# Performance work log

Measured on AMD Instinct MI355X. Metric: run time of the kernel, lower is better.

The kernel has to match this reference:

```python
import math
import jax, jax.numpy as jnp
import numpy as np

B, T, HIDDEN = 2, 2048, 1024
H, HKV, D = 16, 16, 64


def _rope_tables(T, D):
    inv_freq = 1.0 / (10000.0 ** (jnp.arange(0, D, 2, dtype=jnp.float32) / D))
    t = jnp.arange(T, dtype=jnp.float32)
    freqs = jnp.outer(t, inv_freq)               # [T, D/2]
    emb = jnp.concatenate([freqs, freqs], axis=-1)  # [T, D]
    return jnp.cos(emb), jnp.sin(emb)


def setup_inputs() -> dict:
    key = jax.random.key(0)
    k1, k2, k3 = jax.random.split(key, 3)
    hidden_states = jax.random.normal(k1, (B, T, HIDDEN), dtype=jnp.float32)
    cos, sin = _rope_tables(T, D)
    # trunc-normal-ish init, std = 1/sqrt(fan_in)
    w_qkv = jax.random.normal(k2, ((H + 2 * HKV) * D, HIDDEN), dtype=jnp.float32) / math.sqrt(HIDDEN)
    w_o = jax.random.normal(k3, (HIDDEN, H * D), dtype=jnp.float32) / math.sqrt(H * D)
    return {"hidden_states": hidden_states, "cos": cos, "sin": sin, "w_qkv": w_qkv, "w_o": w_o}


def _rotate_half(x):
    x1, x2 = jnp.split(x, 2, axis=-1)
    return jnp.concatenate([-x2, x1], axis=-1)


def reference(hidden_states, cos, sin, w_qkv, w_o):
    b, t, _ = hidden_states.shape
    # fused QKV projection: [B,T,(H+2*HKV)*D]
    qkv = jnp.einsum('bti,oi->bto', hidden_states, w_qkv)
    qkv = qkv.reshape(b, t, H + 2 * HKV, D)
    q = qkv[:, :, :H]                    # [B,T,H,D]
    k = qkv[:, :, H:H + HKV]             # [B,T,HKV,D]
    v = qkv[:, :, H + HKV:]              # [B,T,HKV,D]
    # inline RoPE; cos/sin broadcast over heads
    c = cos[:, None, :]
    s = sin[:, None, :]
    q = q * c + _rotate_half(q) * s
    k = k * c + _rotate_half(k) * s
    scale = 1.0 / math.sqrt(D)
    attn_scores = jnp.einsum('bthd,bThd->bhtT', q, k) * scale  # [B,H,T,T]
    mask = jnp.tril(jnp.ones((t, t), dtype=bool))
    attn_scores = jnp.where(mask[None, None, :, :], attn_scores, -1e9)
    attn = jax.nn.softmax(attn_scores, axis=-1)
    context = jnp.einsum('bhtT,bThd->bthd', attn, v).reshape(b, t, H * D)
    return jnp.einsum('bti,oi->bto', context, w_o)
```

## Files before the change

kernel.cpp:

```cpp
#include <hip/hip_runtime.h>

typedef __bf16 bf16_t;
typedef __bf16 bf16x4 __attribute__((ext_vector_type(4)));
typedef __bf16 bf16x8 __attribute__((ext_vector_type(8)));
typedef float f32x4 __attribute__((ext_vector_type(4)));
typedef unsigned int u32x2 __attribute__((ext_vector_type(2)));
typedef unsigned long long u64;

#define MFMA16(a, b, c) __builtin_amdgcn_mfma_f32_16x16x32_bf16((a), (b), (c), 0, 0, 0)

#define LDG2LDS16(g, l)                                                        \
    __builtin_amdgcn_global_load_lds(                                          \
        (const __attribute__((address_space(1))) void*)(g),                    \
        (__attribute__((address_space(3))) void*)(l), 16, 0, 0)

#if __has_builtin(__builtin_amdgcn_exp2f)
#define EXP2(x) __builtin_amdgcn_exp2f(x)
#else
#define EXP2(x) exp2f(x)
#endif

__device__ inline bf16x8 load8(const float* p) {
    const f32x4 a = *(const f32x4*)p;
    const f32x4 b = *(const f32x4*)(p + 4);
    bf16x8 r;
#pragma unroll
    for (int i = 0; i < 4; i++) { r[i] = (bf16_t)a[i]; r[4 + i] = (bf16_t)b[i]; }
    return r;
}

__device__ inline u32x2 as2(bf16x4 v) {
    u32x2 r;
    __builtin_memcpy(&r, &v, 8);
    return r;
}

__device__ inline bf16x4 shfl4(bf16x4 v, int src) {
    u64 x;
    __builtin_memcpy(&x, &v, 8);
    x = __shfl(x, src, 64);
    bf16x4 r;
    __builtin_memcpy(&r, &x, 8);
    return r;
}

__device__ inline bf16x8 p2pf(bf16x4 pb0, bf16x4 pb1, int quad, int lr) {
    bf16x8 pf;
#if __has_builtin(__builtin_amdgcn_permlane16_swap) && \
    __has_builtin(__builtin_amdgcn_permlane32_swap)
    const u32x2 P0 = as2(pb0);
    const u32x2 P1 = as2(pb1);
    const u32x2 s1a = __builtin_amdgcn_permlane16_swap(P0[0], P0[1], false, false);
    const u32x2 s1b = __builtin_amdgcn_permlane16_swap(P1[0], P1[1], false, false);
    const u32x2 s2a = __builtin_amdgcn_permlane32_swap(s1a[0], s1b[0], false, false);
    const u32x2 s2b = __builtin_amdgcn_permlane32_swap(s1a[1], s1b[1], false, false);
    const u32x2 s3a = __builtin_amdgcn_permlane16_swap(s2a[0], s2a[1], false, false);
    const u32x2 s3b = __builtin_amdgcn_permlane16_swap(s2b[0], s2b[1], false, false);
    const unsigned pfd[4] = {s3a[0], s3a[1], s3b[0], s3b[1]};
    __builtin_memcpy(&pf, pfd, 16);
#else
    const int srcLow = ((quad & 1) << 5) + lr;
    const int srcHigh = srcLow + 16;
    const bool loSel = (quad < 2);
    const bf16x4 a0 = shfl4(pb0, srcLow);
    const bf16x4 a1 = shfl4(pb1, srcLow);
    const bf16x4 b0 = shfl4(pb0, srcHigh);
    const bf16x4 b1 = shfl4(pb1, srcHigh);
    const bf16x4 lo = loSel ? a0 : a1;
    const bf16x4 hi = loSel ? b0 : b1;
#pragma unroll
    for (int r = 0; r < 4; r++) { pf[r] = lo[r]; pf[4 + r] = hi[r]; }
#endif
    return pf;
}

__global__ __launch_bounds__(256) void convert_kernel(const float* __restrict__ hs,
                                                      const float* __restrict__ wqkv,
                                                      const float* __restrict__ wo,
                                                      bf16_t* __restrict__ outb) {
    const size_t c = ((size_t)blockIdx.x * 256 + threadIdx.x) * 8;
    const float* src;
    size_t off;
    if (c < 4194304) { src = hs; off = c; }
    else if (c < 7340032) { src = wqkv; off = c - 4194304; }
    else { src = wo; off = c - 7340032; }
    *(bf16x8*)(outb + c) = load8(src + off);
}


template <int MODE, int NDIM, int BM>
__global__ __launch_bounds__(256) void gemm_bt(const bf16_t* __restrict__ A,
                                               const bf16_t* __restrict__ B,
                                               float* __restrict__ outp,
                                               bf16_t* __restrict__ q_ws,
                                               bf16_t* __restrict__ k_ws,
                                               bf16_t* __restrict__ v_ws,
                                               const float* __restrict__ cosb,
                                               const float* __restrict__ sinb) {
    constexpr int K = 1024;
    constexpr int IM = BM / 32;
    __shared__ __align__(16) bf16_t As[BM * 32];
    __shared__ __align__(16) bf16_t Bs[128 * 32];

    const int tid = threadIdx.x;
    const int w = tid >> 6;
    const int lane = tid & 63;
    const int lr = lane & 15;
    const int quad = lane >> 4;
    const int m0 = blockIdx.y * BM;
    const int n0 = blockIdx.x * 128;
    const int wm = (w & 1) * (BM / 2);
    const int wn = (w >> 1) * 64;

    const int srow = tid >> 2;
    const int skk = (((tid & 3) ^ ((tid >> 3) & 3)) * 8);
    const bf16_t* gA0 = A + (size_t)(m0 + srow) * K + skk;
    const bf16_t* gA1 = gA0 + (size_t)64 * K;
    const bf16_t* gB0 = B + (size_t)(n0 + srow) * K + skk;
    const bf16_t* gB1 = gB0 + (size_t)64 * K;
    bf16_t* lA0 = As + w * 512;
    bf16_t* lA1 = As + 2048 + w * 512;
    bf16_t* lB0 = Bs + w * 512;
    bf16_t* lB1 = Bs + 2048 + w * 512;

    const int qsw = (quad ^ ((lr >> 1) & 3)) * 8;

    f32x4 acc[IM][4] = {};

    for (int k0 = 0; k0 < K; k0 += 32) {
        LDG2LDS16(gA0 + k0, lA0);
        if constexpr (BM == 128) LDG2LDS16(gA1 + k0, lA1);
        LDG2LDS16(gB0 + k0, lB0);
        LDG2LDS16(gB1 + k0, lB1);
        __syncthreads();

        bf16x8 af[IM], bfm[4];
#pragma unroll
        for (int im = 0; im < IM; im++)
            af[im] = *(const bf16x8*)&As[(wm + im * 16 + lr) * 32 + qsw];
#pragma unroll
        for (int in = 0; in < 4; in++)
            bfm[in] = *(const bf16x8*)&Bs[(wn + in * 16 + lr) * 32 + qsw];
#pragma unroll
        for (int im = 0; im < IM; im++)
#pragma unroll
            for (int in = 0; in < 4; in++)
                acc[im][in] = MFMA16(af[im], bfm[in], acc[im][in]);
        __syncthreads();
    }

    if constexpr (MODE == 0) {
#pragma unroll
        for (int im = 0; im < IM; im++)
#pragma unroll
            for (int in = 0; in < 4; in++)
#pragma unroll
                for (int r = 0; r < 4; r++) {
                    const int m = m0 + wm + im * 16 + quad * 4 + r;
                    const int n = n0 + wn + in * 16 + lr;
                    outp[(size_t)m * NDIM + n] = acc[im][in][r];
                }
    } else {
        const int j = (n0 + wn) >> 6;
        if (j < 32) {
            const bool isq = (j < 16);
            const float qs = 0.125f * 1.44269504089f;
#pragma unroll
            for (int im = 0; im < IM; im++) {
#pragma unroll
                for (int r = 0; r < 4; r++) {
                    const int m = m0 + wm + im * 16 + quad * 4 + r;
                    const int b = m >> 11;
                    const int t = m & 2047;
#pragma unroll
                    for (int in = 0; in < 2; in++) {
                        const int d = in * 16 + lr;
                        const float x1 = acc[im][in][r];
                        const float x2 = acc[im][in + 2][r];
                        const float c = cosb[t * 64 + d];
                        const float s = sinb[t * 64 + d];
                        float y1 = x1 * c - x2 * s;
                        float y2 = x2 * c + x1 * s;
                        if (isq) {
                            y1 *= qs; y2 *= qs;
                            const size_t base =
                                ((size_t)(b * 16 + j) * 2048 + t) * 64 + d;
                            q_ws[base] = (bf16_t)y1;
                            q_ws[base + 32] = (bf16_t)y2;
                        } else {
                            const int bh = b * 16 + (j - 16);
                            const size_t off =
                                ((size_t)(bh * 128 + (t >> 4)) * 2) * 512 +
                                ((t & 15) + (d >> 3) * 16) * 8 + (d & 7);
                            k_ws[off] = (bf16_t)y1;
                            k_ws[off + 512] = (bf16_t)y2;
                        }
                    }
                }
            }
        } else {
#pragma unroll
            for (int im = 0; im < IM; im++)
#pragma unroll
                for (int in = 0; in < 4; in++)
#pragma unroll
                    for (int r = 0; r < 4; r++) {
                        const int m = m0 + wm + im * 16 + quad * 4 + r;
                        const int b = m >> 11;
                        const int t = m & 2047;
                        const int d = in * 16 + lr;
                        const int bh = b * 16 + (j - 32);
                        const size_t off =
                            ((size_t)(bh * 64 + (t >> 5)) * 4 + (d >> 4)) * 512 +
                            ((d & 15) + ((t & 31) >> 3) * 16) * 8 + (t & 7);
                        v_ws[off] = (bf16_t)acc[im][in][r];
                    }
        }
    }
}

__global__ __launch_bounds__(512, 4) void attn_kernel(const bf16_t* __restrict__ q_ws,
                                                      const bf16_t* __restrict__ k_ws,
                                                      const bf16_t* __restrict__ v_ws,
                                                      bf16_t* __restrict__ ctx) {
    __shared__ __align__(16) bf16_t Ks[2][4096];
    __shared__ __align__(16) bf16_t Vs[2][4096];

    const int tid = threadIdx.x;
    const int w = tid >> 6;
    const int wq = w & 3;
    const int lane = tid & 63;
    const int lr = lane & 15;
    const int quad = lane >> 4;
    const int bh = blockIdx.x & 31;
    const int g = blockIdx.x >> 5;
    const int pr = (g < 8) ? g : 23 - g;
    const int qtA = pr;
    const int qtB = 31 - pr;
    const int qtw = (w < 4) ? qtA : qtB;
    const int b = bh >> 4;
    const int hd = bh & 15;

    const bf16_t* kws = k_ws + (size_t)bh * 131072;
    const bf16_t* vws = v_ws + (size_t)bh * 131072;
    const int soff = wq * 512 + lane * 8;
    const int lo8 = lane * 8;

    bf16x8 ones8;
#pragma unroll
    for (int i = 0; i < 8; i++) ones8[i] = (bf16_t)1.0f;

#define ASTAGE(kb, bufi)                                                       \
    {                                                                          \
        if (w < 4) {                                                           \
            LDG2LDS16(kws + (size_t)(kb) * 4096 + soff, &Ks[bufi][wq * 512]);  \
            LDG2LDS16(kws + (size_t)(kb) * 4096 + 2048 + soff,                 \
                      &Ks[bufi][2048 + wq * 512]);                             \
        } else {                                                               \
            LDG2LDS16(vws + (size_t)(kb) * 4096 + soff, &Vs[bufi][wq * 512]);  \
            LDG2LDS16(vws + (size_t)(kb) * 4096 + 2048 + soff,                 \
                      &Vs[bufi][2048 + wq * 512]);                             \
        }                                                                      \
    }

    const int trow = qtw * 64 + wq * 16;
    const int query = trow + lr;

    const bf16_t* qb = q_ws + ((size_t)bh * 2048 + trow + lr) * 64 + quad * 8;
    const bf16x8 qlo = *(const bf16x8*)qb;
    const bf16x8 qhi = *(const bf16x8*)(qb + 32);

    f32x4 o[4] = {};
    f32x4 lacc = {};

    ASTAGE(0, 0);
    asm volatile("s_waitcnt vmcnt(0)" ::: "memory");
    __builtin_amdgcn_s_barrier();
    asm volatile("" ::: "memory");

    for (int kb = 0; kb <= qtB; kb++) {
        const int bufi = kb & 1;
        if (kb < qtB) ASTAGE(kb + 1, bufi ^ 1);

        if (kb <= qtw) {
            f32x4 s[4];
#pragma unroll
            for (int n = 0; n < 4; n++) {
                const bf16x8 k0 = *(const bf16x8*)&Ks[bufi][(2 * n) * 512 + lo8];
                const bf16x8 k1 =
                    *(const bf16x8*)&Ks[bufi][(2 * n + 1) * 512 + lo8];
                const f32x4 z = {};
                s[n] = MFMA16(k0, qlo, z);
                s[n] = MFMA16(k1, qhi, s[n]);
            }

            const int u0 = kb * 64;
            if (kb == qtw) {
#pragma unroll
                for (int n = 0; n < 4; n++)
#pragma unroll
                    for (int r = 0; r < 4; r++)
                        if (u0 + n * 16 + quad * 4 + r > query) s[n][r] = -1e9f;
            }

            bf16x4 pb[4];
#pragma unroll
            for (int n = 0; n < 4; n++)
#pragma unroll
                for (int r = 0; r < 4; r++) pb[n][r] = (bf16_t)EXP2(s[n][r]);

#pragma unroll
            for (int hh = 0; hh < 2; hh++) {
                const bf16x8 pf = p2pf(pb[2 * hh], pb[2 * hh + 1], quad, lr);
                lacc = MFMA16(ones8, pf, lacc);
#pragma unroll
                for (int n = 0; n < 4; n++) {
                    const bf16x8 vvf =
                        *(const bf16x8*)&Vs[bufi][(hh * 4 + n) * 512 + lo8];
                    o[n] = MFMA16(vvf, pf, o[n]);
                }
            }
        }

        asm volatile("s_waitcnt lgkmcnt(0) vmcnt(0)" ::: "memory");
        __builtin_amdgcn_s_barrier();
        asm volatile("" ::: "memory");
    }

    const float inv = 1.0f / fmaxf(lacc[0], 1e-30f);
    const size_t base = ((size_t)b * 2048 + query) * 1024 + hd * 64 + quad * 4;
#pragma unroll
    for (int n = 0; n < 4; n++) {
        bf16x4 ob;
#pragma unroll
        for (int r = 0; r < 4; r++) ob[r] = (bf16_t)(o[n][r] * inv);
        *(bf16x4*)&ctx[base + n * 16] = ob;
    }
#undef ASTAGE
}

extern "C" void kernel_launch(void* const* d_in, const int* in_sizes, int n_in,
                              void* d_out, int out_size, void* d_ws, size_t ws_size,
                              hipStream_t stream) {
    const float* hs = (const float*)d_in[0];
    const float* cosb = (const float*)d_in[1];
    const float* sinb = (const float*)d_in[2];
    const float* wqkv = (const float*)d_in[3];
    const float* wo = (const float*)d_in[4];
    float* out = (float*)d_out;

    char* ws = (char*)d_ws;
    bf16_t* hs_b = (bf16_t*)(ws);
    bf16_t* wqkv_b = hs_b + 4194304;
    bf16_t* wo_b = hs_b + 7340032;
    bf16_t* q_ws = (bf16_t*)(ws + (size_t)(16u << 20));
    bf16_t* k_ws = (bf16_t*)(ws + (size_t)(24u << 20));
    bf16_t* v_ws = (bf16_t*)(ws + (size_t)(32u << 20));
    bf16_t* ctx = (bf16_t*)(ws);

    const dim3 blk(256);

    convert_kernel<<<dim3(4096), blk, 0, stream>>>(hs, wqkv, wo, hs_b);

    gemm_bt<1, 3072, 128><<<dim3(24, 32), blk, 0, stream>>>(
        hs_b, wqkv_b, nullptr, q_ws, k_ws, v_ws, cosb, sinb);

    attn_kernel<<<dim3(512), dim3(512), 0, stream>>>(q_ws, k_ws, v_ws, ctx);

    gemm_bt<0, 1024, 64><<<dim3(8, 64), blk, 0, stream>>>(
        ctx, wo_b, out, nullptr, nullptr, nullptr, nullptr, nullptr);
}
```

Measured before the change: 164.8 us.

## Replace QKV GEMM with 512-thread K64 double-buffered async-LDS kernel

Adds a dedicated QKV projection kernel that uses 512 threads, a K-step of 64, and double-buffered global-to-LDS direct loads with XOR-swizzled shared memory and explicit waitcnt/barrier scheduling. Loads for tile t+2 are issued while computing tile t, and MFMA issue is raised in priority with setprio. The goal is to hide global memory latency and halve the number of barrier iterations compared with the old K32 single-buffered GEMM. The cost is more LDS per block (64 KB), which may limit occupancy. The old MODE 1 epilogue is removed from the generic template.

```diff
diff --git a/kernel.cpp b/kernel.cpp
--- a/kernel.cpp
+++ b/kernel.cpp
@@ -88,6 +88,161 @@
 }
 
 
+__global__ __launch_bounds__(512, 4) void gemm1_k64(const bf16_t* __restrict__ A,
+                                                    const bf16_t* __restrict__ B,
+                                                    bf16_t* __restrict__ q_ws,
+                                                    bf16_t* __restrict__ k_ws,
+                                                    bf16_t* __restrict__ v_ws,
+                                                    const float* __restrict__ cosb,
+                                                    const float* __restrict__ sinb) {
+    constexpr int K = 1024;
+    __shared__ __align__(16) bf16_t As[16384];
+    __shared__ __align__(16) bf16_t Bs[16384];
+
+    const int tid = threadIdx.x;
+    const int w = tid >> 6;
+    const int lane = tid & 63;
+    const int lr = lane & 15;
+    const int quad = lane >> 4;
+    const int m0 = blockIdx.y * 128;
+    const int n0 = blockIdx.x * 128;
+    const int wm = (w & 3) * 32;
+    const int wn = (w >> 2) * 64;
+
+    const int trow = tid >> 3;
+    const int slot = (tid & 7) ^ (trow & 7);
+    const bf16_t* gA = A + (size_t)(m0 + trow) * K + slot * 8;
+    const bf16_t* gB = B + (size_t)(n0 + trow) * K + slot * 8;
+
+#define G1STAGE(t, b)                                                          \
+    {                                                                          \
+        LDG2LDS16(gA + (size_t)(t) * 64, As + (b) * 8192 + w * 512);           \
+        LDG2LDS16(gA + (size_t)64 * K + (size_t)(t) * 64,                      \
+                  As + (b) * 8192 + 4096 + w * 512);                           \
+        LDG2LDS16(gB + (size_t)(t) * 64, Bs + (b) * 8192 + w * 512);           \
+        LDG2LDS16(gB + (size_t)64 * K + (size_t)(t) * 64,                      \
+                  Bs + (b) * 8192 + 4096 + w * 512);                           \
+    }
+
+    const int o0 = (quad ^ (lr & 7)) * 16;
+    const char* AbB = (const char*)As + (wm + lr) * 128;
+    const char* BbB = (const char*)Bs + (wn + lr) * 128;
+
+    f32x4 acc[2][4] = {};
+
+    G1STAGE(0, 0);
+    G1STAGE(1, 1);
+    asm volatile("s_waitcnt vmcnt(4)" ::: "memory");
+    __builtin_amdgcn_s_barrier();
+    asm volatile("" ::: "memory");
+
+    for (int t = 0; t < 16; t++) {
+        const int buf = t & 1;
+        const char* pa = AbB + buf * 16384;
+        const char* pb = BbB + buf * 16384;
+        {
+            bf16x8 a0[2], b0[4];
+#pragma unroll
+            for (int im = 0; im < 2; im++)
+                a0[im] = *(const bf16x8*)(pa + im * 2048 + o0);
+#pragma unroll
+            for (int in = 0; in < 4; in++)
+                b0[in] = *(const bf16x8*)(pb + in * 2048 + o0);
+            __builtin_amdgcn_s_setprio(1);
+#pragma unroll
+            for (int im = 0; im < 2; im++)
+#pragma unroll
+                for (int in = 0; in < 4; in++)
+                    acc[im][in] = MFMA16(a0[im], b0[in], acc[im][in]);
+            __builtin_amdgcn_s_setprio(0);
+        }
+        {
+            bf16x8 a1[2], b1[4];
+#pragma unroll
+            for (int im = 0; im < 2; im++)
+                a1[im] = *(const bf16x8*)(pa + im * 2048 + (o0 ^ 64));
+#pragma unroll
+            for (int in = 0; in < 4; in++)
+                b1[in] = *(const bf16x8*)(pb + in * 2048 + (o0 ^ 64));
+            __builtin_amdgcn_s_setprio(1);
+#pragma unroll
+            for (int im = 0; im < 2; im++)
+#pragma unroll
+                for (int in = 0; in < 4; in++)
+                    acc[im][in] = MFMA16(a1[im], b1[in], acc[im][in]);
+            __builtin_amdgcn_s_setprio(0);
+        }
+        asm volatile("s_waitcnt lgkmcnt(0)" ::: "memory");
+        __builtin_amdgcn_s_barrier();
+        asm volatile("" ::: "memory");
+        if (t < 14) {
+            G1STAGE(t + 2, buf);
+            asm volatile("s_waitcnt vmcnt(4)" ::: "memory");
+        } else {
+            asm volatile("s_waitcnt vmcnt(0)" ::: "memory");
+        }
+        __builtin_amdgcn_s_barrier();
+        asm volatile("" ::: "memory");
+    }
+#undef G1STAGE
+
+    const int j = (n0 + wn) >> 6;
+    if (j < 32) {
+        const bool isq = (j < 16);
+        const float qs = 0.125f * 1.44269504089f;
+#pragma unroll
+        for (int im = 0; im < 2; im++) {
+#pragma unroll
+            for (int r = 0; r < 4; r++) {
+                const int m = m0 + wm + im * 16 + quad * 4 + r;
+                const int b = m >> 11;
+                const int t = m & 2047;
+#pragma unroll
+                for (int in = 0; in < 2; in++) {
+                    const int d = in * 16 + lr;
+                    const float x1 = acc[im][in][r];
+                    const float x2 = acc[im][in + 2][r];
+                    const float c = cosb[t * 64 + d];
+                    const float s = sinb[t * 64 + d];
+                    float y1 = x1 * c - x2 * s;
+                    float y2 = x2 * c + x1 * s;
+                    if (isq) {
+                        y1 *= qs; y2 *= qs;
+                        const size_t base =
+                            ((size_t)(b * 16 + j) * 2048 + t) * 64 + d;
+                        q_ws[base] = (bf16_t)y1;
+                        q_ws[base + 32] = (bf16_t)y2;
+                    } else {
+                        const int bh = b * 16 + (j - 16);
+                        const size_t off =
+                            ((size_t)(bh * 128 + (t >> 4)) * 2) * 512 +
+                            ((t & 15) + (d >> 3) * 16) * 8 + (d & 7);
+                        k_ws[off] = (bf16_t)y1;
+                        k_ws[off + 512] = (bf16_t)y2;
+                    }
+                }
+            }
+        }
+    } else {
+#pragma unroll
+        for (int im = 0; im < 2; im++)
+#pragma unroll
+            for (int in = 0; in < 4; in++)
+#pragma unroll
+                for (int r = 0; r < 4; r++) {
+                    const int m = m0 + wm + im * 16 + quad * 4 + r;
+                    const int b = m >> 11;
+                    const int t = m & 2047;
+                    const int d = in * 16 + lr;
+                    const int bh = b * 16 + (j - 32);
+                    const size_t off =
+                        ((size_t)(bh * 64 + (t >> 5)) * 4 + (d >> 4)) * 512 +
+                        ((d & 15) + ((t & 31) >> 3) * 16) * 8 + (t & 7);
+                    v_ws[off] = (bf16_t)acc[im][in][r];
+                }
+    }
+}
+
 template <int MODE, int NDIM, int BM>
 __global__ __launch_bounds__(256) void gemm_bt(const bf16_t* __restrict__ A,
                                                const bf16_t* __restrict__ B,
@@ -161,61 +316,6 @@
                     outp[(size_t)m * NDIM + n] = acc[im][in][r];
                 }
     } else {
-        const int j = (n0 + wn) >> 6;
-        if (j < 32) {
-            const bool isq = (j < 16);
-            const float qs = 0.125f * 1.44269504089f;
-#pragma unroll
-            for (int im = 0; im < IM; im++) {
-#pragma unroll
-                for (int r = 0; r < 4; r++) {
-                    const int m = m0 + wm + im * 16 + quad * 4 + r;
-                    const int b = m >> 11;
-                    const int t = m & 2047;
-#pragma unroll
-                    for (int in = 0; in < 2; in++) {
-                        const int d = in * 16 + lr;
-                        const float x1 = acc[im][in][r];
-                        const float x2 = acc[im][in + 2][r];
-                        const float c = cosb[t * 64 + d];
-                        const float s = sinb[t * 64 + d];
-                        float y1 = x1 * c - x2 * s;
-                        float y2 = x2 * c + x1 * s;
-                        if (isq) {
-                            y1 *= qs; y2 *= qs;
-                            const size_t base =
-                                ((size_t)(b * 16 + j) * 2048 + t) * 64 + d;
-                            q_ws[base] = (bf16_t)y1;
-                            q_ws[base + 32] = (bf16_t)y2;
-                        } else {
-                            const int bh = b * 16 + (j - 16);
-                            const size_t off =
-                                ((size_t)(bh * 128 + (t >> 4)) * 2) * 512 +
-                                ((t & 15) + (d >> 3) * 16) * 8 + (d & 7);
-                            k_ws[off] = (bf16_t)y1;
-                            k_ws[off + 512] = (bf16_t)y2;
-                        }
-                    }
-                }
-            }
-        } else {
-#pragma unroll
-            for (int im = 0; im < IM; im++)
-#pragma unroll
-                for (int in = 0; in < 4; in++)
-#pragma unroll
-                    for (int r = 0; r < 4; r++) {
-                        const int m = m0 + wm + im * 16 + quad * 4 + r;
-                        const int b = m >> 11;
-                        const int t = m & 2047;
-                        const int d = in * 16 + lr;
-                        const int bh = b * 16 + (j - 32);
-                        const size_t off =
-                            ((size_t)(bh * 64 + (t >> 5)) * 4 + (d >> 4)) * 512 +
-                            ((d & 15) + ((t & 31) >> 3) * 16) * 8 + (t & 7);
-                        v_ws[off] = (bf16_t)acc[im][in][r];
-                    }
-        }
     }
 }
 
@@ -362,8 +462,8 @@
 
     convert_kernel<<<dim3(4096), blk, 0, stream>>>(hs, wqkv, wo, hs_b);
 
-    gemm_bt<1, 3072, 128><<<dim3(24, 32), blk, 0, stream>>>(
-        hs_b, wqkv_b, nullptr, q_ws, k_ws, v_ws, cosb, sinb);
+    gemm1_k64<<<dim3(24, 32), dim3(512), 0, stream>>>(
+        hs_b, wqkv_b, q_ws, k_ws, v_ws, cosb, sinb);
 
     attn_kernel<<<dim3(512), dim3(512), 0, stream>>>(q_ws, k_ws, v_ws, ctx);
 
```

Result: no change. 166.1 us (+0.8%).
